# Performance work log

Hardware: AMD Instinct MI355X
Metric: run time of the kernel (lower is better)

Reference implementation:

```python
import jax, jax.numpy as jnp
import numpy as np

GATE_SLOPE = 10.0
ALPHA = 0.8
KH = KW = 3
PAD = 1
STRIDE = 1


def setup_inputs() -> dict:
    key = jax.random.key(0)
    ks = jax.random.split(key, 7)
    B, Cin, H, W = 4, 16, 32, 32
    Cout, NB = 32, 3
    pshape = (Cout, Cin, NB, KH, KW)
    x = jax.random.normal(ks[0], (B, Cin, H, W), dtype=jnp.float32)
    k = jax.random.uniform(ks[1], pshape, dtype=jnp.float32) * 2.0 + 0.5
    Ec = jax.random.uniform(ks[2], pshape, dtype=jnp.float32) * 2.0 + 0.5
    Ps = jax.random.uniform(ks[3], pshape, dtype=jnp.float32) * 1.5 + 0.5
    bias = jax.random.normal(ks[4], pshape, dtype=jnp.float32) * 0.1
    coef = jax.random.normal(ks[5], pshape, dtype=jnp.float32)
    out_bias = jnp.zeros((Cout,), dtype=jnp.float32)
    return {"x": x, "k": k, "Ec": Ec, "Ps": Ps, "bias": bias, "coef": coef, "out_bias": out_bias}


def _unfold(x):
    # x: (B, Cin, H, W) -> (B, Cin, kH, kW, L) like F.unfold with pad/stride
    B, Cin, H, W = x.shape
    Hout = (H + 2 * PAD - KH) // STRIDE + 1
    Wout = (W + 2 * PAD - KW) // STRIDE + 1
    xp = jnp.pad(x, ((0, 0), (0, 0), (PAD, PAD), (PAD, PAD)))
    patches = jnp.stack(
        [xp[:, :, i:i + Hout * STRIDE:STRIDE, j:j + Wout * STRIDE:STRIDE]
         for i in range(KH) for j in range(KW)], axis=2)  # (B,Cin,kH*kW,Hout,Wout)
    return patches.reshape(B, Cin, KH, KW, Hout * Wout), Hout, Wout


def reference(x, k, Ec, Ps, bias, coef, out_bias):
    B, Cin, H, W = x.shape
    Cout = k.shape[0]
    x_exp, Hout, Wout = _unfold(x)  # (B,Cin,kH,kW,L)
    # stateful=False: prev_x = stop_gradient(x), branch = 1.0
    dx = x_exp - jax.lax.stop_gradient(x_exp)
    is_up = jax.nn.sigmoid(GATE_SLOPE * dx)  # value 0.5, nonzero grad path
    # broadcast axes: x -> (B,1,Cin,1,kH,kW,L); params -> (1,Cout,Cin,NB,kH,kW,1)
    x7 = x_exp[:, None, :, None]
    up7 = is_up[:, None, :, None]
    kc, Ecc, Psc, bc, cc = (p[None, ..., None] for p in (k, Ec, Ps, bias, coef))
    crossed_pos = jax.nn.sigmoid(GATE_SLOPE * (x7 - Ecc))
    crossed_neg = jax.nn.sigmoid(GATE_SLOPE * (-x7 - Ecc))
    sw_up = up7 * crossed_pos
    sw_lo = (1.0 - up7) * crossed_neg
    branch = 1.0
    target_sign = sw_up - sw_lo + (1.0 - sw_up - sw_lo) * branch
    branch_momentum = ALPHA * branch + (1.0 - ALPHA) * target_sign
    shifted = x7 + Ecc * branch_momentum
    basis = Psc * jnp.tanh(kc * shifted) + bc
    out = jnp.sum(basis * cc, axis=(2, 3, 4, 5))  # (B,Cout,L)
    out = out.reshape(B, Cout, Hout, Wout) + out_bias[None, :, None, None]
    return out
```

## Files before the change

### kernel.cpp

```cpp
#include <hip/hip_runtime.h>

#define LOG2E 1.4426950408889634f
#define C1 (10.0f * LOG2E)

__global__ __launch_bounds__(256) void prep_kernel(
    const float* __restrict__ x,
    const float* __restrict__ kk, const float* __restrict__ Ec,
    const float* __restrict__ Ps, const float* __restrict__ bias,
    const float* __restrict__ coef, const float* __restrict__ out_bias,
    float2* __restrict__ xe, float4* __restrict__ dp, float* __restrict__ K0) {
    const int bid = blockIdx.x, tid = threadIdx.x;
    if (bid < 289) {
        int i = bid * 256 + tid;
        int ch = i / 1156;
        int rem = i - ch * 1156;
        int r = rem / 34;
        int c = rem - r * 34;
        float xv = 0.f;
        if ((unsigned)(r - 1) < 32u && (unsigned)(c - 1) < 32u)
            xv = x[(ch << 10) + (r - 1) * 32 + (c - 1)];
        xe[i] = make_float2(xv, __builtin_amdgcn_exp2f(C1 * xv));
    } else if (bid < 343) {
        int i = (bid - 289) * 256 + tid;
        int co = i / 432;
        int r  = i - co * 432;
        int ci = r / 27;
        int r2 = r - ci * 27;
        int nb = r2 / 9;
        int j  = r2 - nb * 9;
        int o  = ((co * 16 + ci) * 9 + j) * 3 + nb;
        float e  = Ec[i];
        float zk = 2.0f * LOG2E * kk[i];
        dp[o] = make_float4(__builtin_amdgcn_exp2f(C1 * e), zk, zk * e,
                            2.0f * Ps[i] * coef[i]);
    } else {
        int co = (bid - 343) * 4 + (tid >> 6);
        int lane = tid & 63;
        float sum = 0.f;
        for (int j = lane; j < 432; j += 64) {
            int idx = co * 432 + j;
            sum += coef[idx] * (Ps[idx] + bias[idx]);
        }
        #pragma unroll
        for (int off = 32; off >= 1; off >>= 1) sum += __shfl_down(sum, off, 64);
        if (lane == 0) K0[co] = sum + out_bias[co];
    }
}

__global__ __launch_bounds__(256, 8) void main_kernel(
    const float2* __restrict__ xe, const float4* __restrict__ dp,
    const float* __restrict__ K0, float* __restrict__ out) {
    __shared__ float red[256];
    const int bid = blockIdx.x, tid = threadIdx.x;
    const int chunk = bid & 15;
    const int co    = (bid >> 4) & 31;
    const int b     = bid >> 9;
    const int px = tid & 63;
    const int w  = px & 31;
    const int h  = chunk * 2 + (px >> 5);
    const int cb = __builtin_amdgcn_readfirstlane((int)(tid >> 6)) * 4;

    const float2* xp = xe + ((b * 16 + cb) * 34 + h + 1) * 34 + (w + 1);
    const float4* pk = dp + (co * 16 + cb) * 27;

    float a0 = 0.f, a1 = 0.f, a2 = 0.f;
    float2 X[9], Xn[9];
    #pragma unroll
    for (int j = 0; j < 9; ++j)
        X[j] = xp[(j / 3 - 1) * 34 + (j % 3 - 1)];

    #pragma unroll
    for (int i = 0; i < 4; ++i) {
        if (i < 3) {
            const float2* xn = xp + (i + 1) * 1156;
            #pragma unroll
            for (int j = 0; j < 9; ++j)
                Xn[j] = xn[(j / 3 - 1) * 34 + (j % 3 - 1)];
        }
        const float4* pc = pk + i * 27;
        #pragma unroll
        for (int j = 0; j < 9; ++j) {
            const float xv = X[j].x, E1 = X[j].y;
            const float4 P0 = pc[j * 3 + 0];
            const float4 P1 = pc[j * 3 + 1];
            const float4 P2 = pc[j * 3 + 2];
            float cn0 = __builtin_amdgcn_rcpf(__builtin_fmaf(E1, P0.x, 1.f));
            float cn1 = __builtin_amdgcn_rcpf(__builtin_fmaf(E1, P1.x, 1.f));
            float cn2 = __builtin_amdgcn_rcpf(__builtin_fmaf(E1, P2.x, 1.f));
            float g0 = __builtin_fmaf(-0.2f, cn0, 1.f);
            float g1 = __builtin_fmaf(-0.2f, cn1, 1.f);
            float g2 = __builtin_fmaf(-0.2f, cn2, 1.f);
            float u0 = __builtin_fmaf(P0.y, xv, P0.z * g0);
            float u1 = __builtin_fmaf(P1.y, xv, P1.z * g1);
            float u2 = __builtin_fmaf(P2.y, xv, P2.z * g2);
            float e0 = __builtin_amdgcn_exp2f(u0);
            float e1 = __builtin_amdgcn_exp2f(u1);
            float e2 = __builtin_amdgcn_exp2f(u2);
            float r0 = __builtin_amdgcn_rcpf(1.f + e0);
            float r1 = __builtin_amdgcn_rcpf(1.f + e1);
            float r2 = __builtin_amdgcn_rcpf(1.f + e2);
            a0 = __builtin_fmaf(-P0.w, r0, a0);
            a1 = __builtin_fmaf(-P1.w, r1, a1);
            a2 = __builtin_fmaf(-P2.w, r2, a2);
        }
        #pragma unroll
        for (int j = 0; j < 9; ++j) X[j] = Xn[j];
    }
    red[tid] = a0 + a1 + a2;
    __syncthreads();
    if (tid < 64) {
        float r = red[tid] + red[tid + 64] + red[tid + 128] + red[tid + 192];
        int o = ((b * 32 + co) << 10) + (chunk << 6) + tid;
        out[o] = r + K0[co];
    }
}

extern "C" void kernel_launch(void* const* d_in, const int* in_sizes, int n_in,
                              void* d_out, int out_size, void* d_ws, size_t ws_size,
                              hipStream_t stream) {
    const float* x        = (const float*)d_in[0];
    const float* k        = (const float*)d_in[1];
    const float* Ec       = (const float*)d_in[2];
    const float* Ps       = (const float*)d_in[3];
    const float* bias     = (const float*)d_in[4];
    const float* coef     = (const float*)d_in[5];
    const float* out_bias = (const float*)d_in[6];
    float* out = (float*)d_out;

    float2* xe = (float2*)d_ws;
    float4* dp = (float4*)((char*)d_ws + 73984u * sizeof(float2));
    float*  K0 = (float*)((char*)d_ws + 73984u * sizeof(float2) + 13824u * sizeof(float4));

    prep_kernel<<<351, 256, 0, stream>>>(x, k, Ec, Ps, bias, coef, out_bias, xe, dp, K0);
    main_kernel<<<2048, 256, 0, stream>>>(xe, dp, K0, out);
}
```

Baseline: 30.65 us.

## Stage per-channel parameters in LDS and fold gate constant into precomputed table

Each block now loads the 432 parameter entries for its output channel into shared memory, replacing the per-wave global/scalar loads, and reads them from LDS in the inner loop. The per-element output weight moves to a separate array, and the 0.2*zk*Ec product is precomputed so the inner loop saves one FMA per basis term. Occupancy hint drops from 8 to 6 waves, and a block-wide barrier is added after staging. Previously the parameter reads were wave-uniform scalar loads; they are now LDS reads that may cost more per access than scalar loads.

Result: no change. 30.64 us (-0.0%).

```diff
diff --git a/kernel.cpp b/kernel.cpp
--- a/kernel.cpp
+++ b/kernel.cpp
@@ -8,7 +8,8 @@
     const float* __restrict__ kk, const float* __restrict__ Ec,
     const float* __restrict__ Ps, const float* __restrict__ bias,
     const float* __restrict__ coef, const float* __restrict__ out_bias,
-    float2* __restrict__ xe, float4* __restrict__ dp, float* __restrict__ K0) {
+    float2* __restrict__ xe, float4* __restrict__ P4,
+    float* __restrict__ W2, float* __restrict__ K0) {
     const int bid = blockIdx.x, tid = threadIdx.x;
     if (bid < 289) {
         int i = bid * 256 + tid;
@@ -31,8 +32,9 @@
         int o  = ((co * 16 + ci) * 9 + j) * 3 + nb;
         float e  = Ec[i];
         float zk = 2.0f * LOG2E * kk[i];
-        dp[o] = make_float4(__builtin_amdgcn_exp2f(C1 * e), zk, zk * e,
-                            2.0f * Ps[i] * coef[i]);
+        float a  = zk * e;
+        P4[o] = make_float4(__builtin_amdgcn_exp2f(C1 * e), zk, a, 0.2f * a);
+        W2[o] = 2.0f * Ps[i] * coef[i];
     } else {
         int co = (bid - 343) * 4 + (tid >> 6);
         int lane = tid & 63;
@@ -47,10 +49,13 @@
     }
 }
 
-__global__ __launch_bounds__(256, 8) void main_kernel(
-    const float2* __restrict__ xe, const float4* __restrict__ dp,
-    const float* __restrict__ K0, float* __restrict__ out) {
-    __shared__ float red[256];
+__global__ __launch_bounds__(256, 6) void main_kernel(
+    const float2* __restrict__ xe, const float4* __restrict__ P4,
+    const float* __restrict__ W2, const float* __restrict__ K0,
+    float* __restrict__ out) {
+    __shared__ float4 sP[432];
+    __shared__ float  sW[432];
+    __shared__ float  red[256];
     const int bid = blockIdx.x, tid = threadIdx.x;
     const int chunk = bid & 15;
     const int co    = (bid >> 4) & 31;
@@ -58,17 +63,24 @@
     const int px = tid & 63;
     const int w  = px & 31;
     const int h  = chunk * 2 + (px >> 5);
-    const int cb = __builtin_amdgcn_readfirstlane((int)(tid >> 6)) * 4;
+    const int cb = (tid >> 6) << 2;
+
+    #pragma unroll
+    for (int i = tid; i < 432; i += 256) {
+        sP[i] = P4[co * 432 + i];
+        sW[i] = W2[co * 432 + i];
+    }
 
     const float2* xp = xe + ((b * 16 + cb) * 34 + h + 1) * 34 + (w + 1);
-    const float4* pk = dp + (co * 16 + cb) * 27;
 
-    float a0 = 0.f, a1 = 0.f, a2 = 0.f;
     float2 X[9], Xn[9];
     #pragma unroll
     for (int j = 0; j < 9; ++j)
         X[j] = xp[(j / 3 - 1) * 34 + (j % 3 - 1)];
 
+    __syncthreads();
+
+    float a0 = 0.f, a1 = 0.f, a2 = 0.f;
     #pragma unroll
     for (int i = 0; i < 4; ++i) {
         if (i < 3) {
@@ -77,31 +89,35 @@
             for (int j = 0; j < 9; ++j)
                 Xn[j] = xn[(j / 3 - 1) * 34 + (j % 3 - 1)];
         }
-        const float4* pc = pk + i * 27;
+        const float4* pc = &sP[(cb + i) * 27];
+        const float*  wc = &sW[(cb + i) * 27];
         #pragma unroll
         for (int j = 0; j < 9; ++j) {
             const float xv = X[j].x, E1 = X[j].y;
             const float4 P0 = pc[j * 3 + 0];
             const float4 P1 = pc[j * 3 + 1];
             const float4 P2 = pc[j * 3 + 2];
+            const float w0 = wc[j * 3 + 0];
+            const float w1 = wc[j * 3 + 1];
+            const float w2 = wc[j * 3 + 2];
             float cn0 = __builtin_amdgcn_rcpf(__builtin_fmaf(E1, P0.x, 1.f));
             float cn1 = __builtin_amdgcn_rcpf(__builtin_fmaf(E1, P1.x, 1.f));
             float cn2 = __builtin_amdgcn_rcpf(__builtin_fmaf(E1, P2.x, 1.f));
-            float g0 = __builtin_fmaf(-0.2f, cn0, 1.f);
-            float g1 = __builtin_fmaf(-0.2f, cn1, 1.f);
-            float g2 = __builtin_fmaf(-0.2f, cn2, 1.f);
-            float u0 = __builtin_fmaf(P0.y, xv, P0.z * g0);
-            float u1 = __builtin_fmaf(P1.y, xv, P1.z * g1);
-            float u2 = __builtin_fmaf(P2.y, xv, P2.z * g2);
+            float t0 = __builtin_fmaf(P0.y, xv, P0.z);
+            float t1 = __builtin_fmaf(P1.y, xv, P1.z);
+            float t2 = __builtin_fmaf(P2.y, xv, P2.z);
+            float u0 = __builtin_fmaf(-P0.w, cn0, t0);
+            float u1 = __builtin_fmaf(-P1.w, cn1, t1);
+            float u2 = __builtin_fmaf(-P2.w, cn2, t2);
             float e0 = __builtin_amdgcn_exp2f(u0);
             float e1 = __builtin_amdgcn_exp2f(u1);
             float e2 = __builtin_amdgcn_exp2f(u2);
             float r0 = __builtin_amdgcn_rcpf(1.f + e0);
             float r1 = __builtin_amdgcn_rcpf(1.f + e1);
             float r2 = __builtin_amdgcn_rcpf(1.f + e2);
-            a0 = __builtin_fmaf(-P0.w, r0, a0);
-            a1 = __builtin_fmaf(-P1.w, r1, a1);
-            a2 = __builtin_fmaf(-P2.w, r2, a2);
+            a0 = __builtin_fmaf(-w0, r0, a0);
+            a1 = __builtin_fmaf(-w1, r1, a1);
+            a2 = __builtin_fmaf(-w2, r2, a2);
         }
         #pragma unroll
         for (int j = 0; j < 9; ++j) X[j] = Xn[j];
@@ -128,9 +144,10 @@
     float* out = (float*)d_out;
 
     float2* xe = (float2*)d_ws;
-    float4* dp = (float4*)((char*)d_ws + 73984u * sizeof(float2));
-    float*  K0 = (float*)((char*)d_ws + 73984u * sizeof(float2) + 13824u * sizeof(float4));
+    float4* P4 = (float4*)((char*)d_ws + 591872u);
+    float*  W2 = (float*)((char*)d_ws + 813056u);
+    float*  K0 = (float*)((char*)d_ws + 868352u);
 
-    prep_kernel<<<351, 256, 0, stream>>>(x, k, Ec, Ps, bias, coef, out_bias, xe, dp, K0);
-    main_kernel<<<2048, 256, 0, stream>>>(xe, dp, K0, out);
+    prep_kernel<<<351, 256, 0, stream>>>(x, k, Ec, Ps, bias, coef, out_bias, xe, P4, W2, K0);
+    main_kernel<<<2048, 256, 0, stream>>>(xe, P4, W2, K0, out);
 }
```

## Stage input tile in LDS and batch reciprocals across the three basis terms

Applied to the files above, without the earlier changes.

Each block now copies its 16-channel, 4-row padded input slab into shared memory and reads the 3x3 taps from there, replacing per-thread global loads kept in registers. The inner loop uses a shared-reciprocal trick: the three denominators are multiplied together, one rcp is taken, and each individual reciprocal is rebuilt from partial products. This cuts transcendental rcp calls from six to two per tap. Clamps are added on the denominators and exponents to avoid overflow in the products, at the cost of extra multiplies, some precision risk and an added block barrier.

Result: slower. 38.46 us (+25.5%).

```diff
diff --git a/kernel.cpp b/kernel.cpp
--- a/kernel.cpp
+++ b/kernel.cpp
@@ -8,7 +8,7 @@
     const float* __restrict__ kk, const float* __restrict__ Ec,
     const float* __restrict__ Ps, const float* __restrict__ bias,
     const float* __restrict__ coef, const float* __restrict__ out_bias,
-    float2* __restrict__ xe, float4* __restrict__ dp, float* __restrict__ K0) {
+    float2* __restrict__ xe, float4* __restrict__ P4, float* __restrict__ K0) {
     const int bid = blockIdx.x, tid = threadIdx.x;
     if (bid < 289) {
         int i = bid * 256 + tid;
@@ -31,7 +31,7 @@
         int o  = ((co * 16 + ci) * 9 + j) * 3 + nb;
         float e  = Ec[i];
         float zk = 2.0f * LOG2E * kk[i];
-        dp[o] = make_float4(__builtin_amdgcn_exp2f(C1 * e), zk, zk * e,
+        P4[o] = make_float4(__builtin_amdgcn_exp2f(C1 * e), zk, zk * e,
                             2.0f * Ps[i] * coef[i]);
     } else {
         int co = (bid - 343) * 4 + (tid >> 6);
@@ -48,63 +48,64 @@
 }
 
 __global__ __launch_bounds__(256, 8) void main_kernel(
-    const float2* __restrict__ xe, const float4* __restrict__ dp,
+    const float2* __restrict__ xe, const float4* __restrict__ P4,
     const float* __restrict__ K0, float* __restrict__ out) {
+    __shared__ float2 sX[2176];
     __shared__ float red[256];
     const int bid = blockIdx.x, tid = threadIdx.x;
     const int chunk = bid & 15;
     const int co    = (bid >> 4) & 31;
     const int b     = bid >> 9;
+
+    for (int t = tid; t < 2176; t += 256) {
+        int ci  = t / 136;
+        int rem = t - ci * 136;
+        int r   = rem / 34;
+        int c   = rem - r * 34;
+        sX[t] = xe[((b * 16 + ci) * 34 + chunk * 2 + r) * 34 + c];
+    }
+    __syncthreads();
+
     const int px = tid & 63;
     const int w  = px & 31;
-    const int h  = chunk * 2 + (px >> 5);
-    const int cb = __builtin_amdgcn_readfirstlane((int)(tid >> 6)) * 4;
-
-    const float2* xp = xe + ((b * 16 + cb) * 34 + h + 1) * 34 + (w + 1);
-    const float4* pk = dp + (co * 16 + cb) * 27;
+    const int hr = px >> 5;
+    const int cb = (tid >> 6) << 2;
+    const float4* pk = P4 + (co * 16 + cb) * 27;
 
     float a0 = 0.f, a1 = 0.f, a2 = 0.f;
-    float2 X[9], Xn[9];
-    #pragma unroll
-    for (int j = 0; j < 9; ++j)
-        X[j] = xp[(j / 3 - 1) * 34 + (j % 3 - 1)];
-
     #pragma unroll
     for (int i = 0; i < 4; ++i) {
-        if (i < 3) {
-            const float2* xn = xp + (i + 1) * 1156;
-            #pragma unroll
-            for (int j = 0; j < 9; ++j)
-                Xn[j] = xn[(j / 3 - 1) * 34 + (j % 3 - 1)];
-        }
+        const float2* xw = &sX[(cb + i) * 136 + hr * 34 + w];
         const float4* pc = pk + i * 27;
         #pragma unroll
         for (int j = 0; j < 9; ++j) {
-            const float xv = X[j].x, E1 = X[j].y;
+            const float2 X = xw[(j / 3) * 34 + (j % 3)];
+            const float xv = X.x, E1 = X.y;
             const float4 P0 = pc[j * 3 + 0];
             const float4 P1 = pc[j * 3 + 1];
             const float4 P2 = pc[j * 3 + 2];
-            float cn0 = __builtin_amdgcn_rcpf(__builtin_fmaf(E1, P0.x, 1.f));
-            float cn1 = __builtin_amdgcn_rcpf(__builtin_fmaf(E1, P1.x, 1.f));
-            float cn2 = __builtin_amdgcn_rcpf(__builtin_fmaf(E1, P2.x, 1.f));
-            float g0 = __builtin_fmaf(-0.2f, cn0, 1.f);
-            float g1 = __builtin_fmaf(-0.2f, cn1, 1.f);
-            float g2 = __builtin_fmaf(-0.2f, cn2, 1.f);
-            float u0 = __builtin_fmaf(P0.y, xv, P0.z * g0);
-            float u1 = __builtin_fmaf(P1.y, xv, P1.z * g1);
-            float u2 = __builtin_fmaf(P2.y, xv, P2.z * g2);
+            float d0 = fminf(__builtin_fmaf(E1, P0.x, 1.f), 0x1p25f);
+            float d1 = fminf(__builtin_fmaf(E1, P1.x, 1.f), 0x1p25f);
+            float d2 = fminf(__builtin_fmaf(E1, P2.x, 1.f), 0x1p25f);
+            float q01 = d0 * d1, q12 = d1 * d2, q02 = d0 * d2;
+            float rp  = __builtin_amdgcn_rcpf(q01 * d2);
+            float rp2 = 0.2f * rp;
+            float t0 = __builtin_fmaf(P0.y, xv, P0.z);
+            float t1 = __builtin_fmaf(P1.y, xv, P1.z);
+            float t2 = __builtin_fmaf(P2.y, xv, P2.z);
+            float u0 = fminf(__builtin_fmaf(-P0.z, rp2 * q12, t0), 25.f);
+            float u1 = fminf(__builtin_fmaf(-P1.z, rp2 * q02, t1), 25.f);
+            float u2 = fminf(__builtin_fmaf(-P2.z, rp2 * q01, t2), 25.f);
             float e0 = __builtin_amdgcn_exp2f(u0);
             float e1 = __builtin_amdgcn_exp2f(u1);
             float e2 = __builtin_amdgcn_exp2f(u2);
-            float r0 = __builtin_amdgcn_rcpf(1.f + e0);
-            float r1 = __builtin_amdgcn_rcpf(1.f + e1);
-            float r2 = __builtin_amdgcn_rcpf(1.f + e2);
-            a0 = __builtin_fmaf(-P0.w, r0, a0);
-            a1 = __builtin_fmaf(-P1.w, r1, a1);
-            a2 = __builtin_fmaf(-P2.w, r2, a2);
+            float f0 = 1.f + e0, f1 = 1.f + e1, f2 = 1.f + e2;
+            float s01 = f0 * f1, s12 = f1 * f2, s02 = f0 * f2;
+            float rq  = __builtin_amdgcn_rcpf(s01 * f2);
+            a0 = __builtin_fmaf(-P0.w, rq * s12, a0);
+            a1 = __builtin_fmaf(-P1.w, rq * s02, a1);
+            a2 = __builtin_fmaf(-P2.w, rq * s01, a2);
         }
-        #pragma unroll
-        for (int j = 0; j < 9; ++j) X[j] = Xn[j];
     }
     red[tid] = a0 + a1 + a2;
     __syncthreads();
@@ -128,9 +129,9 @@
     float* out = (float*)d_out;
 
     float2* xe = (float2*)d_ws;
-    float4* dp = (float4*)((char*)d_ws + 73984u * sizeof(float2));
-    float*  K0 = (float*)((char*)d_ws + 73984u * sizeof(float2) + 13824u * sizeof(float4));
+    float4* P4 = (float4*)((char*)d_ws + 591872u);
+    float*  K0 = (float*)((char*)d_ws + 813056u);
 
-    prep_kernel<<<351, 256, 0, stream>>>(x, k, Ec, Ps, bias, coef, out_bias, xe, dp, K0);
-    main_kernel<<<2048, 256, 0, stream>>>(xe, dp, K0, out);
+    prep_kernel<<<351, 256, 0, stream>>>(x, k, Ec, Ps, bias, coef, out_bias, xe, P4, K0);
+    main_kernel<<<2048, 256, 0, stream>>>(xe, P4, K0, out);
 }
```
